# Optimization experiments

Hardware: AMD Instinct MI355X
Metric: run time of the kernel (lower is better)

## Reference

```python
import jax, jax.numpy as jnp
import numpy as np

N_NODES = 50000
N_EDGES = 800000
IN_DIM = 128
EMB_DIM = 128
NUM_LAYER = 3
NUM_GRAPHS = 512
BN_EPS = 1e-5


def setup_inputs() -> dict:
    key = jax.random.key(0)
    ks = jax.random.split(key, 10)
    x = jax.random.normal(ks[0], (N_NODES, IN_DIM), jnp.float32)
    edge_index = jax.random.randint(ks[1], (2, N_EDGES), 0, N_NODES)
    batch = jnp.sort(jax.random.randint(ks[2], (N_NODES,), 0, NUM_GRAPHS))
    W = jax.random.normal(ks[3], (NUM_LAYER, EMB_DIM, EMB_DIM), jnp.float32) / np.sqrt(EMB_DIM)
    b_hidden = 0.01 * jax.random.normal(ks[4], (NUM_LAYER - 1, EMB_DIM), jnp.float32)
    bn_gamma = 1.0 + 0.1 * jax.random.normal(ks[5], (NUM_LAYER, EMB_DIM), jnp.float32)
    bn_beta = 0.1 * jax.random.normal(ks[6], (NUM_LAYER, EMB_DIM), jnp.float32)
    bn_mean = 0.1 * jax.random.normal(ks[7], (NUM_LAYER, EMB_DIM), jnp.float32)
    bn_var = jnp.ones((NUM_LAYER, EMB_DIM), jnp.float32)
    We = jax.random.normal(ks[8], (2 * EMB_DIM, 1), jnp.float32) / np.sqrt(2 * EMB_DIM)
    be = jnp.zeros((1,), jnp.float32)
    Wn = jax.random.normal(ks[9], (EMB_DIM, 1), jnp.float32) / np.sqrt(EMB_DIM)
    bn_bias = jnp.zeros((1,), jnp.float32)
    return dict(x=x, edge_index=edge_index, batch=batch, num_graphs=NUM_GRAPHS,
                W=W, b_hidden=b_hidden, bn_gamma=bn_gamma, bn_beta=bn_beta,
                bn_mean=bn_mean, bn_var=bn_var, We=We, be=be, Wn=Wn, bn_bias=bn_bias)


def batch_norm(x, gamma, beta, mean, var):
    # eval-mode BatchNorm1d with running stats
    return (x - mean) * jax.lax.rsqrt(var + BN_EPS) * gamma + beta


def gcn_propagate(h, edge_index, num_nodes):
    # symmetric-normalized GCN aggregation with self loops (edge_weight = 1)
    loop = jnp.arange(num_nodes)
    row = jnp.concatenate([edge_index[0], loop])
    col = jnp.concatenate([edge_index[1], loop])
    deg = jax.ops.segment_sum(jnp.ones(row.shape[0], h.dtype), row, num_segments=num_nodes)
    dis = jnp.where(deg > 0, jax.lax.rsqrt(jnp.maximum(deg, 1.0)), 0.0)
    norm = dis[row] * dis[col]  # [E+N]
    return jax.ops.segment_sum(norm[:, None] * h[row], col, num_segments=num_nodes)


def reg_mask(mask, seg, size):
    # mask: [S,1]; seg: [S] int segment ids; size graphs
    key_num = jax.ops.segment_sum(mask, seg, num_segments=size) + 1e-8
    env_num = jax.ops.segment_sum(1.0 - mask, seg, num_segments=size) + 1e-8
    non_zero = jax.ops.segment_sum((mask > 0).astype(jnp.float32), seg, num_segments=size)
    all_mask = jax.ops.segment_sum(jnp.ones_like(mask), seg, num_segments=size)
    return key_num, env_num, non_zero / all_mask


def _forward(x, W, b_hidden, bn_gamma, bn_beta, bn_mean, bn_var, We, be, Wn, bn_bias,
             edge_index, batch, num_graphs):
    N = x.shape[0]
    # layer 1: GCNConv(gfn=True) => BN then plain linear (no bias, no propagation)
    h = batch_norm(x, bn_gamma[0], bn_beta[0], bn_mean[0], bn_var[0]) @ W[0]
    h = jax.nn.relu(h)  # num_layer > 1; dropout is identity in eval
    n_hidden = W.shape[0] - 1
    for i in range(n_hidden):
        hb = batch_norm(h, bn_gamma[i + 1], bn_beta[i + 1], bn_mean[i + 1], bn_var[i + 1])
        h = gcn_propagate(hb @ W[i + 1], edge_index, N) + b_hidden[i]
        if i != n_hidden - 1:
            h = jax.nn.relu(h)
    node_rep = h  # [N, emb]

    row, col = edge_index[0], edge_index[1]
    D = node_rep.shape[1]
    node_key = jax.nn.sigmoid(node_rep @ Wn + bn_bias)  # [N,1]
    # cat([rep[row], rep[col]]) @ We == rep[row] @ We[:D] + rep[col] @ We[D:]
    edge_key = jax.nn.sigmoid(node_rep[row] @ We[:D] + node_rep[col] @ We[D:] + be)  # [E,1]

    node_key_num, node_env_num, nz_node_ratio = reg_mask(node_key, batch, num_graphs)
    edge_key_num, edge_env_num, nz_edge_ratio = reg_mask(edge_key, batch[row], num_graphs)
    return (node_key, edge_key, node_key_num, node_env_num,
            edge_key_num, edge_env_num, nz_node_ratio, nz_edge_ratio)


def reference(x, edge_index, batch, num_graphs, W, b_hidden, bn_gamma, bn_beta,
              bn_mean, bn_var, We, be, Wn, bn_bias):
    return _forward(x, W, b_hidden, bn_gamma, bn_beta, bn_mean, bn_var,
                    We, be, Wn, bn_bias, edge_index, batch, num_graphs)
```

## Files before the change

### kernel.cpp

```cpp
#include <hip/hip_runtime.h>
#include <cstddef>
#include <cstring>

#define NN 50000
#define NNP 50048
#define NE 800000
#define D 128
#define NG 512
#define BN_EPS 1e-5f
#define RSZC 25000
#define RSZF 12500
#define NCHUNK 64
#define CSZ 12500
#define EDGE_BLOCKS 256

typedef __bf16 bf16_t;
typedef __bf16 bf16x8 __attribute__((ext_vector_type(8)));
typedef float f32x4 __attribute__((ext_vector_type(4)));

#define OFF_ACCN 0
#define OFF_ACCE 2048
#define OFF_CTR  4096
#define ZERO_FLOATS 4160
#define OFF_DIS  4160
#define OFF_CNT  54208
#define OFF_COLP 104256
#define OFF_ENDS 154304
#define OFF_BSUM 204352
#define OFF_T1   204800
#define OFF_T2   254848
#define OFF_BP   304896
#define OFF_WPT  305408
#define OFF_PR   329984
#define OFF_PC   3533056
#define OFF_SRCS OFF_PR
#define OFF_HBFA 7536128
#define OFF_HBFB 10739200

#define O_NKEY 0
#define O_EKEY 50000
#define O_NKN  850000
#define O_NEN  850512
#define O_EKN  851024
#define O_EEN  851536
#define O_NZN  852048
#define O_NZE  852560

__device__ __forceinline__ float sigmoidf(float x) {
    return 1.0f / (1.0f + expf(-x));
}

__device__ __forceinline__ unsigned short f2bf_bits(float f) {
    bf16_t h = (bf16_t)f;
    unsigned short u;
    __builtin_memcpy(&u, &h, 2);
    return u;
}

__device__ __forceinline__ float bf_lo(unsigned int u) {
    return __uint_as_float(u << 16);
}
__device__ __forceinline__ float bf_hi(unsigned int u) {
    return __uint_as_float(u & 0xFFFF0000u);
}

__global__ __launch_bounds__(256) void count_prep(const int* __restrict__ ei,
                                                  int* __restrict__ PR,
                                                  int* __restrict__ PC,
                                                  const float* __restrict__ W,
                                                  const float* __restrict__ gamma,
                                                  const float* __restrict__ beta,
                                                  const float* __restrict__ mean,
                                                  const float* __restrict__ var,
                                                  bf16_t* __restrict__ Wpt,
                                                  float* __restrict__ bp) {
    const int tid = threadIdx.x;
    if (blockIdx.z == 2) {
        if (blockIdx.x == 0 && blockIdx.y < 3 && tid < D) {
            int l = blockIdx.y;
            int j = tid;
            float acc = 0.f;
            for (int k = 0; k < D; ++k) {
                float a = gamma[l * D + k] * rsqrtf(var[l * D + k] + BN_EPS);
                float c = beta[l * D + k] - mean[l * D + k] * a;
                float w = W[l * D * D + k * D + j];
                Wpt[l * D * D + j * D + k] = (bf16_t)(a * w);
                acc = fmaf(c, w, acc);
            }
            bp[l * D + j] = acc;
        }
        return;
    }
    extern __shared__ int hist[];
    const int r = blockIdx.x, p = blockIdx.y, dirz = blockIdx.z;
    for (int i = tid; i < RSZC; i += 256) hist[i] = 0;
    __syncthreads();
    const int base = r * RSZC;
    const int4* ids = (const int4*)(ei + dirz * NE + p * CSZ);
    for (int i = tid; i < CSZ / 4; i += 256) {
        int4 v = ids[i];
        int d0 = v.x - base, d1 = v.y - base, d2 = v.z - base, d3 = v.w - base;
        if ((unsigned)d0 < RSZC) atomicAdd(&hist[d0], 1);
        if ((unsigned)d1 < RSZC) atomicAdd(&hist[d1], 1);
        if ((unsigned)d2 < RSZC) atomicAdd(&hist[d2], 1);
        if ((unsigned)d3 < RSZC) atomicAdd(&hist[d3], 1);
    }
    __syncthreads();
    int* dst = (dirz == 0 ? PR : PC) + p * NNP + base;
    for (int i = tid; i < RSZC; i += 256) dst[i] = hist[i];
}

__global__ void csr_mid(const int* __restrict__ PR, int* __restrict__ PC,
                        float* __restrict__ dis, int* __restrict__ cnt,
                        int* __restrict__ colp, int* __restrict__ bsum) {
    __shared__ int s[256];
    int t = threadIdx.x;
    int i = blockIdx.x * 256 + t;
    int run = 0;
    if (i < NN) {
        int dg = 0;
#pragma unroll 8
        for (int k = 0; k < NCHUNK; ++k) dg += PR[k * NNP + i];
        dis[i] = rsqrtf((float)(dg + 1));
        for (int k = 0; k < NCHUNK; ++k) {
            int v = PC[k * NNP + i];
            PC[k * NNP + i] = run;
            run += v;
        }
        cnt[i] = run;
    }
    s[t] = run;
    __syncthreads();
    for (int o = 1; o < 256; o <<= 1) {
        int add = (t >= o) ? s[t - o] : 0;
        __syncthreads();
        s[t] += add;
        __syncthreads();
    }
    if (i < NN) colp[i] = s[t] - run;
    if (t == 255) bsum[blockIdx.x] = s[255];
}

__global__ void scan3(int* __restrict__ colp, const int* __restrict__ bsum,
                      const int* __restrict__ cnt, int* __restrict__ ends) {
    __shared__ int s[256];
    int t = threadIdx.x;
    int bid = blockIdx.x;
    s[t] = (t < bid) ? bsum[t] : 0;
    __syncthreads();
    for (int o = 128; o; o >>= 1) {
        if (t < o) s[t] += s[t + o];
        __syncthreads();
    }
    int boff = s[0];
    int i = bid * 256 + t;
    if (i < NN) {
        int v = colp[i] + boff;
        colp[i] = v;
        ends[i] = v + cnt[i];
    }
}

__global__ __launch_bounds__(256) void fill_part(const int* __restrict__ ei,
                                                 const int* __restrict__ colp,
                                                 const int* __restrict__ CPS,
                                                 const float* __restrict__ dis,
                                                 unsigned int* __restrict__ srcs) {
    __shared__ int curs[RSZF];
    const int r = blockIdx.x, p = blockIdx.y;
    const int tid = threadIdx.x;
    const int base = r * RSZF;
    for (int i = tid; i < RSZF; i += 256)
        curs[i] = colp[base + i] + CPS[p * NNP + base + i];
    __syncthreads();
    const int4* rows = (const int4*)(ei + p * CSZ);
    const int4* cols = (const int4*)(ei + NE + p * CSZ);
    for (int i = tid; i < CSZ / 4; i += 256) {
        int4 rv = rows[i];
        int4 cv = cols[i];
        int d;
        d = cv.x - base;
        if ((unsigned)d < RSZF)
            srcs[atomicAdd(&curs[d], 1)] =
                (unsigned int)rv.x | ((unsigned int)f2bf_bits(dis[rv.x]) << 16);
        d = cv.y - base;
        if ((unsigned)d < RSZF)
            srcs[atomicAdd(&curs[d], 1)] =
                (unsigned int)rv.y | ((unsigned int)f2bf_bits(dis[rv.y]) << 16);
        d = cv.z - base;
        if ((unsigned)d < RSZF)
            srcs[atomicAdd(&curs[d], 1)] =
                (unsigned int)rv.z | ((unsigned int)f2bf_bits(dis[rv.z]) << 16);
        d = cv.w - base;
        if ((unsigned)d < RSZF)
            srcs[atomicAdd(&curs[d], 1)] =
                (unsigned int)rv.w | ((unsigned int)f2bf_bits(dis[rv.w]) << 16);
    }
}

__global__ __launch_bounds__(256) void gemm01(const float* __restrict__ X,
                                              const bf16_t* __restrict__ Bt0,
                                              const bf16_t* __restrict__ Bt1,
                                              const float* __restrict__ bias0,
                                              const float* __restrict__ bias1,
                                              bf16_t* __restrict__ out) {
    extern __shared__ __align__(16) unsigned short smem[];
    unsigned short* Bs0 = smem;
    unsigned short* Bs1 = smem + 16384;
    unsigned short* As  = smem + 32768;
    const int tid = threadIdx.x;
    const int wv = tid >> 6;
    const int lane = tid & 63;
    const int l15 = lane & 15;
    const int l4 = lane >> 4;
    const int row0 = blockIdx.x * 64;

    for (int q = tid; q < 2048; q += 256) {
        int r = q >> 4, u = q & 15;
        int us = (u ^ (r & 7)) * 8;
        *(uint4*)&Bs0[r * 128 + us] = *(const uint4*)(Bt0 + r * D + u * 8);
        *(uint4*)&Bs1[r * 128 + us] = *(const uint4*)(Bt1 + r * D + u * 8);
    }

    bf16x8 afrag[4];
    {
        int r = row0 + wv * 16 + l15;
        int rc = (r < NN) ? r : (NN - 1);
#pragma unroll
        for (int kk = 0; kk < 4; ++kk) {
            int off = rc * D + kk * 32 + l4 * 8;
            float4 f0 = *(const float4*)(X + off);
            float4 f1 = *(const float4*)(X + off + 4);
            bf16x8 a;
            a[0] = (bf16_t)f0.x; a[1] = (bf16_t)f0.y;
            a[2] = (bf16_t)f0.z; a[3] = (bf16_t)f0.w;
            a[4] = (bf16_t)f1.x; a[5] = (bf16_t)f1.y;
            a[6] = (bf16_t)f1.z; a[7] = (bf16_t)f1.w;
            afrag[kk] = a;
        }
    }
    __syncthreads();

    const int rsw = l15 & 7;
    f32x4 acc[8];
#pragma unroll
    for (int n = 0; n < 8; ++n) acc[n] = (f32x4){0.f, 0.f, 0.f, 0.f};
#pragma unroll
    for (int n = 0; n < 8; ++n) {
#pragma unroll
        for (int kk = 0; kk < 4; ++kk) {
            bf16x8 bfrag = *(const bf16x8*)&Bs0[(n * 16 + l15) * 128 + ((kk * 4 + l4) ^ rsw) * 8];
            acc[n] = __builtin_amdgcn_mfma_f32_16x16x32_bf16(afrag[kk], bfrag, acc[n], 0, 0, 0);
        }
    }
#pragma unroll
    for (int n = 0; n < 8; ++n) {
        int col = n * 16 + l15;
        float bv = bias0[col];
#pragma unroll
        for (int r = 0; r < 4; ++r) {
            int rl = wv * 16 + l4 * 4 + r;
            float v = fmaxf(acc[n][r] + bv, 0.f);
            int cs = ((col >> 3) ^ (rl & 7));
            As[rl * 128 + cs * 8 + (col & 7)] = f2bf_bits(v);
        }
    }
    __syncthreads();

    const int rl = wv * 16 + l15;
    bf16x8 af2[4];
#pragma unroll
    for (int kk = 0; kk < 4; ++kk) {
        int cs = (kk * 4 + l4) ^ (rl & 7);
        af2[kk] = *(const bf16x8*)&As[rl * 128 + cs * 8];
    }
#pragma unroll
    for (int n = 0; n < 8; ++n) acc[n] = (f32x4){0.f, 0.f, 0.f, 0.f};
#pragma unroll
    for (int n = 0; n < 8; ++n) {
#pragma unroll
        for (int kk = 0; kk < 4; ++kk) {
            bf16x8 bfrag = *(const bf16x8*)&Bs1[(n * 16 + l15) * 128 + ((kk * 4 + l4) ^ rsw) * 8];
            acc[n] = __builtin_amdgcn_mfma_f32_16x16x32_bf16(af2[kk], bfrag, acc[n], 0, 0, 0);
        }
    }
#pragma unroll
    for (int n = 0; n < 8; ++n) {
        int col = n * 16 + l15;
        float bv = bias1[col];
#pragma unroll
        for (int r = 0; r < 4; ++r) {
            int row = row0 + wv * 16 + l4 * 4 + r;
            if (row < NN) out[(size_t)row * D + col] = (bf16_t)(acc[n][r] + bv);
        }
    }
}

__global__ __launch_bounds__(256) void gemm2(const bf16_t* __restrict__ A,
                                             const bf16_t* __restrict__ Bt,
                                             const float* __restrict__ bias,
                                             bf16_t* __restrict__ out) {
    __shared__ __align__(16) unsigned short Bs[128 * 128];
    const int tid = threadIdx.x;
    const int wv = tid >> 6;
    const int lane = tid & 63;
    const int l15 = lane & 15;
    const int l4 = lane >> 4;
    const int row0 = blockIdx.x * 64 + wv * 16;

    for (int q = tid; q < 2048; q += 256) {
        int r = q >> 4, u = q & 15;
        *(uint4*)&Bs[r * 128 + (u ^ (r & 7)) * 8] = *(const uint4*)(Bt + r * D + u * 8);
    }

    bf16x8 afrag[4];
    {
        int r = row0 + l15;
        int rc = (r < NN) ? r : (NN - 1);
#pragma unroll
        for (int kk = 0; kk < 4; ++kk)
            afrag[kk] = *(const bf16x8*)(A + rc * D + kk * 32 + l4 * 8);
    }
    __syncthreads();

    const int rsw = l15 & 7;
    f32x4 acc[8];
#pragma unroll
    for (int n = 0; n < 8; ++n) acc[n] = (f32x4){0.f, 0.f, 0.f, 0.f};
#pragma unroll
    for (int n = 0; n < 8; ++n) {
#pragma unroll
        for (int kk = 0; kk < 4; ++kk) {
            bf16x8 bfrag = *(const bf16x8*)&Bs[(n * 16 + l15) * 128 + ((kk * 4 + l4) ^ rsw) * 8];
            acc[n] = __builtin_amdgcn_mfma_f32_16x16x32_bf16(afrag[kk], bfrag, acc[n], 0, 0, 0);
        }
    }
#pragma unroll
    for (int n = 0; n < 8; ++n) {
        int col = n * 16 + l15;
        float bv = bias[col];
#pragma unroll
        for (int r = 0; r < 4; ++r) {
            int row = row0 + l4 * 4 + r;
            if (row < NN) out[(size_t)row * D + col] = (bf16_t)(acc[n][r] + bv);
        }
    }
}

template <int POST>
__global__ __launch_bounds__(256) void prop_gather(
    const int* __restrict__ colp, const int* __restrict__ ends,
    const unsigned int* __restrict__ srcs, const float* __restrict__ dis,
    const bf16_t* __restrict__ hin, bf16_t* __restrict__ hout,
    const float* __restrict__ bias) {
    int n = blockIdx.x * 4 + (threadIdx.x >> 6);
    n = __builtin_amdgcn_readfirstlane(n);
    int lane = threadIdx.x & 63;
    if (n >= NN) return;
    const int start = colp[n];
    const int end = ends[n];
    const float dn = dis[n];
    unsigned int u = ((const unsigned int*)(hin + (size_t)n * D))[lane];
    float ax = dn * bf_lo(u), ay = dn * bf_hi(u);
    int i = start;
    for (; i + 3 < end; i += 4) {
        unsigned int e0 = srcs[i], e1 = srcs[i + 1], e2 = srcs[i + 2], e3 = srcs[i + 3];
        unsigned int u0 = ((const unsigned int*)(hin + (size_t)(e0 & 0xFFFFu) * D))[lane];
        unsigned int u1 = ((const unsigned int*)(hin + (size_t)(e1 & 0xFFFFu) * D))[lane];
        unsigned int u2 = ((const unsigned int*)(hin + (size_t)(e2 & 0xFFFFu) * D))[lane];
        unsigned int u3 = ((const unsigned int*)(hin + (size_t)(e3 & 0xFFFFu) * D))[lane];
        float w0 = bf_hi(e0), w1 = bf_hi(e1), w2 = bf_hi(e2), w3 = bf_hi(e3);
        ax = fmaf(w0, bf_lo(u0), ax); ay = fmaf(w0, bf_hi(u0), ay);
        ax = fmaf(w1, bf_lo(u1), ax); ay = fmaf(w1, bf_hi(u1), ay);
        ax = fmaf(w2, bf_lo(u2), ax); ay = fmaf(w2, bf_hi(u2), ay);
        ax = fmaf(w3, bf_lo(u3), ax); ay = fmaf(w3, bf_hi(u3), ay);
    }
    for (; i < end; ++i) {
        unsigned int e0 = srcs[i];
        unsigned int u0 = ((const unsigned int*)(hin + (size_t)(e0 & 0xFFFFu) * D))[lane];
        float w0 = bf_hi(e0);
        ax = fmaf(w0, bf_lo(u0), ax); ay = fmaf(w0, bf_hi(u0), ay);
    }
    float vx = dn * ax, vy = dn * ay;
    if (POST == 0) {
        float2 bb = ((const float2*)bias)[lane];
        vx = fmaxf(vx + bb.x, 0.f);
        vy = fmaxf(vy + bb.y, 0.f);
    }
    unsigned int pk = (unsigned int)f2bf_bits(vx) | ((unsigned int)f2bf_bits(vy) << 16);
    ((unsigned int*)(hout + (size_t)n * D))[lane] = pk;
}

__global__ __launch_bounds__(256) void node_kernel(
    const bf16_t* __restrict__ h, const float* __restrict__ bh1,
    const float* __restrict__ We, const float* __restrict__ Wn,
    const float* __restrict__ bnb, const int* __restrict__ batch,
    float* __restrict__ nkey_out, float* __restrict__ t1, float* __restrict__ t2,
    float* __restrict__ accN) {
    __shared__ float binK[NG], binE[NG], binZ[NG], binC[NG];
    const int tid = threadIdx.x;
    for (int i = tid; i < NG; i += 256) { binK[i] = 0.f; binE[i] = 0.f; binZ[i] = 0.f; binC[i] = 0.f; }
    __syncthreads();

    const int CHUNK = 98;
    int start = blockIdx.x * CHUNK;
    int end = min(start + CHUNK, NN);
    int sub = tid >> 5;
    int l32 = tid & 31;
    float bnb0 = bnb[0];

    float4 w1 = ((const float4*)We)[l32];
    float4 w2 = ((const float4*)(We + D))[l32];
    float4 wn = ((const float4*)Wn)[l32];
    float4 bb = ((const float4*)bh1)[l32];

    for (int n = start + sub; n < end; n += 8) {
        uint2 pk = ((const uint2*)(h + (size_t)n * D))[l32];
        float v0 = bf_lo(pk.x) + bb.x;
        float v1 = bf_hi(pk.x) + bb.y;
        float v2 = bf_lo(pk.y) + bb.z;
        float v3 = bf_hi(pk.y) + bb.w;
        float s1 = v0 * w1.x + v1 * w1.y + v2 * w1.z + v3 * w1.w;
        float s2 = v0 * w2.x + v1 * w2.y + v2 * w2.z + v3 * w2.w;
        float s3 = v0 * wn.x + v1 * wn.y + v2 * wn.z + v3 * wn.w;
        for (int o = 16; o; o >>= 1) {
            s1 += __shfl_xor(s1, o);
            s2 += __shfl_xor(s2, o);
            s3 += __shfl_xor(s3, o);
        }
        if (l32 == 0) {
            t1[n] = s1;
            t2[n] = s2;
            float nk = sigmoidf(s3 + bnb0);
            nkey_out[n] = nk;
            int g = batch[n];
            atomicAdd(&binK[g], nk);
            atomicAdd(&binE[g], 1.0f - nk);
            if (nk > 0.f) atomicAdd(&binZ[g], 1.0f);
            atomicAdd(&binC[g], 1.0f);
        }
    }
    __syncthreads();
    if (start < NN) {
        int glo = batch[start];
        int ghi = batch[end - 1];
        for (int g = glo + tid; g <= ghi; g += 256) {
            unsafeAtomicAdd(&accN[g], binK[g]);
            unsafeAtomicAdd(&accN[NG + g], binE[g]);
            unsafeAtomicAdd(&accN[2 * NG + g], binZ[g]);
            unsafeAtomicAdd(&accN[3 * NG + g], binC[g]);
        }
    }
}

__global__ __launch_bounds__(256) void edge_final(
    const int* __restrict__ ei, const float* __restrict__ t1,
    const float* __restrict__ t2, const float* __restrict__ be,
    const int* __restrict__ batch, float* __restrict__ ekey_out,
    float* __restrict__ accE, const float* __restrict__ accN,
    int* __restrict__ ctr, float* __restrict__ out) {
    __shared__ float binK[NG], binE[NG], binZ[NG], binC[NG];
    __shared__ int isLast;
    const int tid = threadIdx.x;
    for (int i = tid; i < NG; i += 256) { binK[i] = 0.f; binE[i] = 0.f; binZ[i] = 0.f; binC[i] = 0.f; }
    __syncthreads();
    float be0 = be[0];
    int stride4 = gridDim.x * 256;
    for (int q = blockIdx.x * 256 + tid; q < NE / 4; q += stride4) {
        int4 r4 = ((const int4*)ei)[q];
        int4 c4 = ((const int4*)(ei + NE))[q];
        float a0 = t1[r4.x], a1 = t1[r4.y], a2 = t1[r4.z], a3 = t1[r4.w];
        float b0 = t2[c4.x], b1 = t2[c4.y], b2 = t2[c4.z], b3 = t2[c4.w];
        int g0 = batch[r4.x], g1 = batch[r4.y], g2 = batch[r4.z], g3 = batch[r4.w];
        float e0 = sigmoidf(a0 + b0 + be0);
        float e1 = sigmoidf(a1 + b1 + be0);
        float e2 = sigmoidf(a2 + b2 + be0);
        float e3 = sigmoidf(a3 + b3 + be0);
        ((float4*)ekey_out)[q] = make_float4(e0, e1, e2, e3);
        atomicAdd(&binK[g0], e0); atomicAdd(&binE[g0], 1.0f - e0);
        if (e0 > 0.f) atomicAdd(&binZ[g0], 1.0f);
        atomicAdd(&binC[g0], 1.0f);
        atomicAdd(&binK[g1], e1); atomicAdd(&binE[g1], 1.0f - e1);
        if (e1 > 0.f) atomicAdd(&binZ[g1], 1.0f);
        atomicAdd(&binC[g1], 1.0f);
        atomicAdd(&binK[g2], e2); atomicAdd(&binE[g2], 1.0f - e2);
        if (e2 > 0.f) atomicAdd(&binZ[g2], 1.0f);
        atomicAdd(&binC[g2], 1.0f);
        atomicAdd(&binK[g3], e3); atomicAdd(&binE[g3], 1.0f - e3);
        if (e3 > 0.f) atomicAdd(&binZ[g3], 1.0f);
        atomicAdd(&binC[g3], 1.0f);
    }
    __syncthreads();
    for (int g = tid; g < NG; g += 256) {
        if (binC[g] != 0.f) {
            unsafeAtomicAdd(&accE[g], binK[g]);
            unsafeAtomicAdd(&accE[NG + g], binE[g]);
            unsafeAtomicAdd(&accE[2 * NG + g], binZ[g]);
            unsafeAtomicAdd(&accE[3 * NG + g], binC[g]);
        }
    }
    __syncthreads();
    if (tid == 0) {
        __threadfence();
        int old = atomicAdd(ctr, 1);
        isLast = (old == (int)gridDim.x - 1);
    }
    __syncthreads();
    if (isLast) {
        __threadfence();
        for (int g = tid; g < NG; g += 256) {
            out[O_NKN + g] = accN[g] + 1e-8f;
            out[O_NEN + g] = accN[NG + g] + 1e-8f;
            out[O_EKN + g] = accE[g] + 1e-8f;
            out[O_EEN + g] = accE[NG + g] + 1e-8f;
            out[O_NZN + g] = accN[2 * NG + g] / accN[3 * NG + g];
            out[O_NZE + g] = accE[2 * NG + g] / accE[3 * NG + g];
        }
    }
}

extern "C" void kernel_launch(void* const* d_in, const int* in_sizes, int n_in,
                              void* d_out, int out_size, void* d_ws, size_t ws_size,
                              hipStream_t stream) {
    const float* x     = (const float*)d_in[0];
    const int*   ei    = (const int*)d_in[1];
    const int*   batch = (const int*)d_in[2];
    const float* W     = (const float*)d_in[4];
    const float* bh    = (const float*)d_in[5];
    const float* gamma = (const float*)d_in[6];
    const float* beta  = (const float*)d_in[7];
    const float* mean  = (const float*)d_in[8];
    const float* var   = (const float*)d_in[9];
    const float* We    = (const float*)d_in[10];
    const float* be    = (const float*)d_in[11];
    const float* Wn    = (const float*)d_in[12];
    const float* bnb   = (const float*)d_in[13];

    float* ws  = (float*)d_ws;
    float* out = (float*)d_out;

    float*        accN = ws + OFF_ACCN;
    float*        accE = ws + OFF_ACCE;
    int*          ctr  = (int*)(ws + OFF_CTR);
    float*        dis  = ws + OFF_DIS;
    int*          cnt  = (int*)(ws + OFF_CNT);
    int*          colp = (int*)(ws + OFF_COLP);
    int*          ends = (int*)(ws + OFF_ENDS);
    int*          bsum = (int*)(ws + OFF_BSUM);
    float*        t1   = ws + OFF_T1;
    float*        t2   = ws + OFF_T2;
    float*        bp   = ws + OFF_BP;
    bf16_t*       Wpt  = (bf16_t*)(ws + OFF_WPT);
    int*          PR   = (int*)(ws + OFF_PR);
    int*          PC   = (int*)(ws + OFF_PC);
    unsigned int* srcs = (unsigned int*)(ws + OFF_SRCS);
    bf16_t*       hbfA = (bf16_t*)(ws + OFF_HBFA);
    bf16_t*       hbfB = (bf16_t*)(ws + OFF_HBFB);

    hipMemsetAsync(d_ws, 0, (size_t)ZERO_FLOATS * sizeof(float), stream);

    count_prep<<<dim3(2, NCHUNK, 3), 256, RSZC * sizeof(int), stream>>>(
        ei, PR, PC, W, gamma, beta, mean, var, Wpt, bp);
    const int NB = (NN + 255) / 256;
    csr_mid<<<NB, 256, 0, stream>>>(PR, PC, dis, cnt, colp, bsum);
    scan3<<<NB, 256, 0, stream>>>(colp, bsum, cnt, ends);
    fill_part<<<dim3(4, NCHUNK), 256, 0, stream>>>(ei, colp, PC, dis, srcs);

    const int GB = (NN + 63) / 64;
    gemm01<<<GB, 256, 81920, stream>>>(x, Wpt, Wpt + D * D, bp, bp + D, hbfB);
    prop_gather<0><<<12500, 256, 0, stream>>>(colp, ends, srcs, dis, hbfB, hbfA, bh);
    gemm2<<<GB, 256, 0, stream>>>(hbfA, Wpt + 2 * D * D, bp + 2 * D, hbfB);
    prop_gather<1><<<12500, 256, 0, stream>>>(colp, ends, srcs, dis, hbfB, hbfA, nullptr);

    node_kernel<<<512, 256, 0, stream>>>(hbfA, bh + D, We, Wn, bnb, batch,
                                         out + O_NKEY, t1, t2, accN);
    edge_final<<<EDGE_BLOCKS, 256, 0, stream>>>(ei, t1, t2, be, batch,
                                                out + O_EKEY, accE, accN, ctr, out);
}
```

Baseline: 214.6 us.

## Fuse CSR fill into gemm01 launch and pack edge lookup data into float4

Merges the fill_part kernel into the first GEMM kernel as 256 extra blocks, so the CSR fill and the layer-0/1 GEMM run concurrently in one launch. The two are independent, so this removes a launch boundary and lets the two phases overlap. It also packs t1, t2 and the graph id per node into one float4, so edge_final does one 16-byte gather per endpoint instead of separate t1, t2 and batch gathers. The cost is that fill blocks now reserve 80KB of dynamic shared memory, which lowers their occupancy, and the packed table gathers more bytes than edge_final actually uses.

```diff
diff --git a/kernel.cpp b/kernel.cpp
--- a/kernel.cpp
+++ b/kernel.cpp
@@ -27,13 +27,12 @@
 #define OFF_COLP 104256
 #define OFF_ENDS 154304
 #define OFF_BSUM 204352
-#define OFF_T1   204800
-#define OFF_T2   254848
 #define OFF_BP   304896
 #define OFF_WPT  305408
 #define OFF_PR   329984
 #define OFF_PC   3533056
 #define OFF_SRCS OFF_PR
+#define OFF_TB   1129984
 #define OFF_HBFA 7536128
 #define OFF_HBFB 10739200
 
@@ -161,59 +160,58 @@
     }
 }
 
-__global__ __launch_bounds__(256) void fill_part(const int* __restrict__ ei,
-                                                 const int* __restrict__ colp,
-                                                 const int* __restrict__ CPS,
-                                                 const float* __restrict__ dis,
-                                                 unsigned int* __restrict__ srcs) {
-    __shared__ int curs[RSZF];
-    const int r = blockIdx.x, p = blockIdx.y;
+__global__ __launch_bounds__(256) void fill_gemm01(
+    const int* __restrict__ ei, const int* __restrict__ colp,
+    const int* __restrict__ CPS, const float* __restrict__ dis,
+    unsigned int* __restrict__ srcs,
+    const float* __restrict__ X, const bf16_t* __restrict__ Bt0,
+    const bf16_t* __restrict__ Bt1, const float* __restrict__ bias0,
+    const float* __restrict__ bias1, bf16_t* __restrict__ out) {
+    extern __shared__ __align__(16) unsigned short smem[];
+    const int bid = blockIdx.x;
     const int tid = threadIdx.x;
-    const int base = r * RSZF;
-    for (int i = tid; i < RSZF; i += 256)
-        curs[i] = colp[base + i] + CPS[p * NNP + base + i];
-    __syncthreads();
-    const int4* rows = (const int4*)(ei + p * CSZ);
-    const int4* cols = (const int4*)(ei + NE + p * CSZ);
-    for (int i = tid; i < CSZ / 4; i += 256) {
-        int4 rv = rows[i];
-        int4 cv = cols[i];
-        int d;
-        d = cv.x - base;
-        if ((unsigned)d < RSZF)
-            srcs[atomicAdd(&curs[d], 1)] =
-                (unsigned int)rv.x | ((unsigned int)f2bf_bits(dis[rv.x]) << 16);
-        d = cv.y - base;
-        if ((unsigned)d < RSZF)
-            srcs[atomicAdd(&curs[d], 1)] =
-                (unsigned int)rv.y | ((unsigned int)f2bf_bits(dis[rv.y]) << 16);
-        d = cv.z - base;
-        if ((unsigned)d < RSZF)
-            srcs[atomicAdd(&curs[d], 1)] =
-                (unsigned int)rv.z | ((unsigned int)f2bf_bits(dis[rv.z]) << 16);
-        d = cv.w - base;
-        if ((unsigned)d < RSZF)
-            srcs[atomicAdd(&curs[d], 1)] =
-                (unsigned int)rv.w | ((unsigned int)f2bf_bits(dis[rv.w]) << 16);
-    }
-}
-
-__global__ __launch_bounds__(256) void gemm01(const float* __restrict__ X,
-                                              const bf16_t* __restrict__ Bt0,
-                                              const bf16_t* __restrict__ Bt1,
-                                              const float* __restrict__ bias0,
-                                              const float* __restrict__ bias1,
-                                              bf16_t* __restrict__ out) {
-    extern __shared__ __align__(16) unsigned short smem[];
+
+    if (bid < 256) {
+        int* curs = (int*)smem;
+        const int r = bid & 3, p = bid >> 2;
+        const int base = r * RSZF;
+        for (int i = tid; i < RSZF; i += 256)
+            curs[i] = colp[base + i] + CPS[p * NNP + base + i];
+        __syncthreads();
+        const int4* rows = (const int4*)(ei + p * CSZ);
+        const int4* cols = (const int4*)(ei + NE + p * CSZ);
+        for (int i = tid; i < CSZ / 4; i += 256) {
+            int4 rv = rows[i];
+            int4 cv = cols[i];
+            int d;
+            d = cv.x - base;
+            if ((unsigned)d < RSZF)
+                srcs[atomicAdd(&curs[d], 1)] =
+                    (unsigned int)rv.x | ((unsigned int)f2bf_bits(dis[rv.x]) << 16);
+            d = cv.y - base;
+            if ((unsigned)d < RSZF)
+                srcs[atomicAdd(&curs[d], 1)] =
+                    (unsigned int)rv.y | ((unsigned int)f2bf_bits(dis[rv.y]) << 16);
+            d = cv.z - base;
+            if ((unsigned)d < RSZF)
+                srcs[atomicAdd(&curs[d], 1)] =
+                    (unsigned int)rv.z | ((unsigned int)f2bf_bits(dis[rv.z]) << 16);
+            d = cv.w - base;
+            if ((unsigned)d < RSZF)
+                srcs[atomicAdd(&curs[d], 1)] =
+                    (unsigned int)rv.w | ((unsigned int)f2bf_bits(dis[rv.w]) << 16);
+        }
+        return;
+    }
+
     unsigned short* Bs0 = smem;
     unsigned short* Bs1 = smem + 16384;
     unsigned short* As  = smem + 32768;
-    const int tid = threadIdx.x;
     const int wv = tid >> 6;
     const int lane = tid & 63;
     const int l15 = lane & 15;
     const int l4 = lane >> 4;
-    const int row0 = blockIdx.x * 64;
+    const int row0 = (bid - 256) * 64;
 
     for (int q = tid; q < 2048; q += 256) {
         int r = q >> 4, u = q & 15;
@@ -395,7 +393,7 @@
     const bf16_t* __restrict__ h, const float* __restrict__ bh1,
     const float* __restrict__ We, const float* __restrict__ Wn,
     const float* __restrict__ bnb, const int* __restrict__ batch,
-    float* __restrict__ nkey_out, float* __restrict__ t1, float* __restrict__ t2,
+    float* __restrict__ nkey_out, float4* __restrict__ tb,
     float* __restrict__ accN) {
     __shared__ float binK[NG], binE[NG], binZ[NG], binC[NG];
     const int tid = threadIdx.x;
@@ -429,11 +427,10 @@
             s3 += __shfl_xor(s3, o);
         }
         if (l32 == 0) {
-            t1[n] = s1;
-            t2[n] = s2;
             float nk = sigmoidf(s3 + bnb0);
             nkey_out[n] = nk;
             int g = batch[n];
+            tb[n] = make_float4(s1, s2, __int_as_float(g), 0.f);
             atomicAdd(&binK[g], nk);
             atomicAdd(&binE[g], 1.0f - nk);
             if (nk > 0.f) atomicAdd(&binZ[g], 1.0f);
@@ -454,9 +451,8 @@
 }
 
 __global__ __launch_bounds__(256) void edge_final(
-    const int* __restrict__ ei, const float* __restrict__ t1,
-    const float* __restrict__ t2, const float* __restrict__ be,
-    const int* __restrict__ batch, float* __restrict__ ekey_out,
+    const int* __restrict__ ei, const float4* __restrict__ tb,
+    const float* __restrict__ be, float* __restrict__ ekey_out,
     float* __restrict__ accE, const float* __restrict__ accN,
     int* __restrict__ ctr, float* __restrict__ out) {
     __shared__ float binK[NG], binE[NG], binZ[NG], binC[NG];
@@ -469,13 +465,14 @@
     for (int q = blockIdx.x * 256 + tid; q < NE / 4; q += stride4) {
         int4 r4 = ((const int4*)ei)[q];
         int4 c4 = ((const int4*)(ei + NE))[q];
-        float a0 = t1[r4.x], a1 = t1[r4.y], a2 = t1[r4.z], a3 = t1[r4.w];
-        float b0 = t2[c4.x], b1 = t2[c4.y], b2 = t2[c4.z], b3 = t2[c4.w];
-        int g0 = batch[r4.x], g1 = batch[r4.y], g2 = batch[r4.z], g3 = batch[r4.w];
-        float e0 = sigmoidf(a0 + b0 + be0);
-        float e1 = sigmoidf(a1 + b1 + be0);
-        float e2 = sigmoidf(a2 + b2 + be0);
-        float e3 = sigmoidf(a3 + b3 + be0);
+        float4 tr0 = tb[r4.x], tr1 = tb[r4.y], tr2 = tb[r4.z], tr3 = tb[r4.w];
+        float4 tc0 = tb[c4.x], tc1 = tb[c4.y], tc2 = tb[c4.z], tc3 = tb[c4.w];
+        int g0 = __float_as_int(tr0.z), g1 = __float_as_int(tr1.z);
+        int g2 = __float_as_int(tr2.z), g3 = __float_as_int(tr3.z);
+        float e0 = sigmoidf(tr0.x + tc0.y + be0);
+        float e1 = sigmoidf(tr1.x + tc1.y + be0);
+        float e2 = sigmoidf(tr2.x + tc2.y + be0);
+        float e3 = sigmoidf(tr3.x + tc3.y + be0);
         ((float4*)ekey_out)[q] = make_float4(e0, e1, e2, e3);
         atomicAdd(&binK[g0], e0); atomicAdd(&binE[g0], 1.0f - e0);
         if (e0 > 0.f) atomicAdd(&binZ[g0], 1.0f);
@@ -547,13 +544,12 @@
     int*          colp = (int*)(ws + OFF_COLP);
     int*          ends = (int*)(ws + OFF_ENDS);
     int*          bsum = (int*)(ws + OFF_BSUM);
-    float*        t1   = ws + OFF_T1;
-    float*        t2   = ws + OFF_T2;
     float*        bp   = ws + OFF_BP;
     bf16_t*       Wpt  = (bf16_t*)(ws + OFF_WPT);
     int*          PR   = (int*)(ws + OFF_PR);
     int*          PC   = (int*)(ws + OFF_PC);
     unsigned int* srcs = (unsigned int*)(ws + OFF_SRCS);
+    float4*       tb   = (float4*)(ws + OFF_TB);
     bf16_t*       hbfA = (bf16_t*)(ws + OFF_HBFA);
     bf16_t*       hbfB = (bf16_t*)(ws + OFF_HBFB);
 
@@ -564,16 +560,16 @@
     const int NB = (NN + 255) / 256;
     csr_mid<<<NB, 256, 0, stream>>>(PR, PC, dis, cnt, colp, bsum);
     scan3<<<NB, 256, 0, stream>>>(colp, bsum, cnt, ends);
-    fill_part<<<dim3(4, NCHUNK), 256, 0, stream>>>(ei, colp, PC, dis, srcs);
 
     const int GB = (NN + 63) / 64;
-    gemm01<<<GB, 256, 81920, stream>>>(x, Wpt, Wpt + D * D, bp, bp + D, hbfB);
+    fill_gemm01<<<256 + GB, 256, 81920, stream>>>(ei, colp, PC, dis, srcs,
+                                                  x, Wpt, Wpt + D * D, bp, bp + D, hbfB);
     prop_gather<0><<<12500, 256, 0, stream>>>(colp, ends, srcs, dis, hbfB, hbfA, bh);
     gemm2<<<GB, 256, 0, stream>>>(hbfA, Wpt + 2 * D * D, bp + 2 * D, hbfB);
     prop_gather<1><<<12500, 256, 0, stream>>>(colp, ends, srcs, dis, hbfB, hbfA, nullptr);
 
     node_kernel<<<512, 256, 0, stream>>>(hbfA, bh + D, We, Wn, bnb, batch,
-                                         out + O_NKEY, t1, t2, accN);
-    edge_final<<<EDGE_BLOCKS, 256, 0, stream>>>(ei, t1, t2, be, batch,
-                                                out + O_EKEY, accE, accN, ctr, out);
-}
+                                         out + O_NKEY, tb, accN);
+    edge_final<<<EDGE_BLOCKS, 256, 0, stream>>>(ei, tb, be, out + O_EKEY,
+                                                accE, accN, ctr, out);
+}
```

Result: faster. 204.9 us (-4.5%).
